# Performance work log

Hardware: AMD Instinct MI355X
Metric: run time of the kernel (lower is better)

The kernel has to match this reference:

```python
import jax, jax.numpy as jnp
import numpy as np

B, I, H = 8192, 1024, 1024


def setup_inputs() -> dict:
    key = jax.random.key(0)
    k1, k2, k3, k4, k5 = jax.random.split(key, 5)
    bound_in = 1.0 / np.sqrt(I)
    return {
        "input": jax.random.normal(k1, (B, I), dtype=jnp.float32),
        "weights": jax.random.uniform(k2, (4 * H, H + I), dtype=jnp.float32, minval=-bound_in, maxval=bound_in),
        "bias": jax.random.uniform(k3, (4 * H,), dtype=jnp.float32, minval=-bound_in, maxval=bound_in),
        "old_h": jax.random.normal(k4, (B, H), dtype=jnp.float32),
        "old_cell": jax.random.normal(k5, (B, H), dtype=jnp.float32),
    }


def reference(input, weights, bias, old_h, old_cell):
    # X = [old_h, input] matches weights = cat(recurrent_W, input_W, dim=1)
    X = jnp.concatenate([old_h, input], axis=1)            # [B, H+I]
    gates = jax.nn.sigmoid(X @ weights.T + bias)           # [B, 4H], all gates sigmoid
    in_g, out_g, z_g, f_g = jnp.split(gates, 4, axis=1)    # each [B, H]
    new_cell = old_cell * f_g + z_g - in_g                 # subtractive cell update
    new_h = jax.nn.sigmoid(new_cell) - out_g               # subtractive output
    return new_h, new_cell
```

## Files before the change

kernel.cpp:

```cpp
#include <hip/hip_runtime.h>
#include <hip/hip_bf16.h>

namespace {

constexpr int kB = 8192;
constexpr int kH = 1024;
constexpr int kK = 2048;
constexpr int kG = 4 * kH;

typedef float f32x4 __attribute__((ext_vector_type(4)));
typedef unsigned short u16x8 __attribute__((ext_vector_type(8)));

__device__ __forceinline__ unsigned short f2bf(float f) {
  return __builtin_bit_cast(unsigned short, __float2bfloat16(f));
}
__device__ __forceinline__ float sigmoidf_(float x) {
  return 1.0f / (1.0f + __expf(-x));
}
__device__ __forceinline__ u16x8 pack8(const float4 v0, const float4 v1) {
  return u16x8{f2bf(v0.x), f2bf(v0.y), f2bf(v0.z), f2bf(v0.w),
               f2bf(v1.x), f2bf(v1.y), f2bf(v1.z), f2bf(v1.w)};
}

__global__ __launch_bounds__(256) void prep_pack(
    const float* __restrict__ input, const float* __restrict__ weights,
    const float* __restrict__ bias, const float* __restrict__ old_h,
    unsigned short* __restrict__ Aw, unsigned short* __restrict__ Ww,
    float* __restrict__ bias_i) {
  const int b = blockIdx.x;
  const int tid = threadIdx.x;

  if (b >= 3072) {
    const int base = (b - 3072) * 2048 + tid * 8;
    #pragma unroll
    for (int e = 0; e < 8; ++e) {
      const int j = base + e;
      bias_i[j] = bias[(j & 3) * kH + (j >> 2)];
    }
    return;
  }

  __shared__ unsigned short tile[8192];

  const bool isW = (b >= 2048);
  const int tileid = isW ? (b - 2048) : b;
  const int kt  = tileid & 31;
  const int blk = tileid >> 5;

  const int r    = tid >> 1;
  const int half = tid & 1;
  const int k0   = kt * 64 + half * 32;

  const float* src;
  if (!isW) {
    const int row = blk * 128 + r;
    src = (k0 < kH) ? (old_h + (long)row * kH + k0)
                    : (input + (long)row * kH + (k0 - kH));
  } else {
    const int j = blk * 128 + r;
    const int g = j & 3, h = j >> 2;
    src = weights + ((long)g * kH + h) * kK + k0;
  }

  float4 v[8];
  const float4* s4 = (const float4*)src;
  #pragma unroll
  for (int q = 0; q < 8; ++q) v[q] = s4[q];

  const int mb = r >> 4, r15 = r & 15;
  #pragma unroll
  for (int lh = 0; lh < 4; ++lh) {
    const int dst = mb * 1024 + half * 512 + (lh * 16 + r15) * 8;
    *(u16x8*)&tile[dst] = pack8(v[2 * lh], v[2 * lh + 1]);
  }
  __syncthreads();

  unsigned short* out = (isW ? Ww : Aw) + (long)tileid * 8192;
  #pragma unroll
  for (int q = 0; q < 4; ++q)
    *(u16x8*)(out + q * 2048 + tid * 8) = *(const u16x8*)&tile[q * 2048 + tid * 8];
}

__global__ __launch_bounds__(256, 2) void sublstm_gemm(
    const unsigned short* __restrict__ Aw, const unsigned short* __restrict__ Ww,
    const float* __restrict__ bias_i, const float* __restrict__ old_cell,
    float* __restrict__ out) {

  __shared__ union SM {
    struct { unsigned short A0[8192]; unsigned short B0[8192];
             unsigned short A1[8192]; unsigned short B1[8192]; } t;
    float Gc[32][132];
  } sm;
  __shared__ float bias_s[128];

  const int tid  = threadIdx.x;
  const int lane = tid & 63;
  const int wid  = tid >> 6;
  const int wr   = wid >> 1;
  const int wc   = wid & 1;

  const int bid = blockIdx.x;
  const int swz = (bid & 7) * 256 + (bid >> 3);
  const int bm  = swz & 63;
  const int hb  = swz >> 6;

  if (tid < 128) bias_s[tid] = bias_i[hb * 128 + tid];

  const unsigned short* atile = Aw + ((long)bm * 32) * 8192;
  const unsigned short* btile = Ww + ((long)hb * 32) * 8192;
  const int soff = tid * 8;

  unsigned short* A0 = sm.t.A0; unsigned short* B0 = sm.t.B0;
  unsigned short* A1 = sm.t.A1; unsigned short* B1 = sm.t.B1;

  f32x4 acc[4][4];
  #pragma unroll
  for (int m = 0; m < 4; ++m)
    #pragma unroll
    for (int n = 0; n < 4; ++n)
      acc[m][n] = f32x4{0.f, 0.f, 0.f, 0.f};

#define STAGE(LA, LB, KT) do {                                                     \
    const unsigned short* asrc_ = atile + (long)(KT) * 8192 + soff;                \
    const unsigned short* bsrc_ = btile + (long)(KT) * 8192 + soff;                \
    _Pragma("unroll")                                                              \
    for (int i_ = 0; i_ < 4; ++i_) {                                               \
      __builtin_amdgcn_global_load_lds(                                            \
          (const __attribute__((address_space(1))) unsigned int*)(asrc_ + i_ * 2048), \
          (__attribute__((address_space(3))) unsigned int*)((LA) + i_ * 2048 + wid * 512), \
          16, 0, 0);                                                               \
      __builtin_amdgcn_global_load_lds(                                            \
          (const __attribute__((address_space(1))) unsigned int*)(bsrc_ + i_ * 2048), \
          (__attribute__((address_space(3))) unsigned int*)((LB) + i_ * 2048 + wid * 512), \
          16, 0, 0);                                                               \
    }                                                                              \
  } while (0)

#define COMPUTE(LA, LB) do {                                                       \
    _Pragma("unroll")                                                              \
    for (int kk_ = 0; kk_ < 2; ++kk_) {                                            \
      u16x8 af_[4], bf_[4];                                                        \
      _Pragma("unroll")                                                            \
      for (int m_ = 0; m_ < 4; ++m_)                                               \
        af_[m_] = *(const u16x8*)&(LA)[((wr * 4 + m_) * 2 + kk_) * 512 + lane * 8];\
      _Pragma("unroll")                                                            \
      for (int n_ = 0; n_ < 4; ++n_)                                               \
        bf_[n_] = *(const u16x8*)&(LB)[((wc * 4 + n_) * 2 + kk_) * 512 + lane * 8];\
      _Pragma("unroll")                                                            \
      for (int m_ = 0; m_ < 4; ++m_)                                               \
        _Pragma("unroll")                                                          \
        for (int n_ = 0; n_ < 4; ++n_)                                             \
          asm("v_mfma_f32_16x16x32_bf16 %0, %1, %2, %0"                            \
              : "+v"(acc[m_][n_]) : "v"(af_[m_]), "v"(bf_[n_]));                   \
    }                                                                              \
  } while (0)

  STAGE(A0, B0, 0);
  __syncthreads();

  for (int kt = 0; kt + 2 < 32; kt += 2) {
    STAGE(A1, B1, kt + 1);
    COMPUTE(A0, B0);
    __syncthreads();
    STAGE(A0, B0, kt + 2);
    COMPUTE(A1, B1);
    __syncthreads();
  }
  STAGE(A1, B1, 31);

  float ocp[4][4];
  #pragma unroll
  for (int m = 0; m < 4; ++m)
    #pragma unroll
    for (int q = 0; q < 4; ++q) {
      const int r = (tid >> 5) + q * 8;
      const int grow = bm * 128 + (r >> 4) * 64 + m * 16 + (r & 15);
      ocp[m][q] = old_cell[(long)grow * kH + hb * 32 + (tid & 31)];
    }

  COMPUTE(A0, B0);
  __syncthreads();
  COMPUTE(A1, B1);

#undef STAGE
#undef COMPUTE

  float* out_h = out;
  float* out_c = out + (long)kB * kH;

  #pragma unroll
  for (int m = 0; m < 4; ++m) {
    __syncthreads();
    #pragma unroll
    for (int n = 0; n < 4; ++n) {
      const int col = wc * 64 + n * 16 + (lane & 15);
      #pragma unroll
      for (int j = 0; j < 4; ++j)
        sm.Gc[wr * 16 + (lane >> 4) * 4 + j][col] = acc[m][n][j];
    }
    __syncthreads();

    #pragma unroll
    for (int q = 0; q < 4; ++q) {
      const int r = (tid >> 5) + q * 8;
      const int h = tid & 31;
      const float4 gv = *(const float4*)&sm.Gc[r][h * 4];
      const float4 bv = *(const float4*)&bias_s[h * 4];
      const float gi = sigmoidf_(gv.x + bv.x);
      const float go = sigmoidf_(gv.y + bv.y);
      const float gz = sigmoidf_(gv.z + bv.z);
      const float gf = sigmoidf_(gv.w + bv.w);
      const int grow = bm * 128 + (r >> 4) * 64 + m * 16 + (r & 15);
      const long off = (long)grow * kH + hb * 32 + h;
      const float nc = ocp[m][q] * gf + gz - gi;
      out_h[off] = sigmoidf_(nc) - go;
      out_c[off] = nc;
    }
  }
}

constexpr int FBM = 128, FBH = 32, FBN = 128, FBK = 32, FNKT = kK / FBK;

__global__ __launch_bounds__(256, 2) void sublstm_fused(
    const float* __restrict__ input, const float* __restrict__ weights,
    const float* __restrict__ bias, const float* __restrict__ old_h,
    const float* __restrict__ old_cell, float* __restrict__ out) {
  __shared__ unsigned short As[FBM][FBK + 8];
  __shared__ unsigned short Bs[FBN][FBK + 8];
  __shared__ float Gc[32][FBN + 4];

  const int tid = threadIdx.x, lane = tid & 63, wid = tid >> 6;
  const int wr = wid >> 1, wc = wid & 1;
  const int bid = blockIdx.x;
  const int bm = bid & 63, hh0 = (bid >> 6) * FBH;

  const int ra = tid >> 1, ca = (tid & 1) << 4;
  const long arow = (long)bm * FBM + ra;
  const int wrow = (ra >> 5) * kH + hh0 + (ra & 31);
  const float* abase_h = old_h + arow * kH + ca;
  const float* abase_x = input + arow * kH + ca - kH;
  const float* wbase = weights + (long)wrow * kK + ca;

  const int fr = lane & 15, ks = (lane >> 4) << 3;
  f32x4 acc[4][4];
  #pragma unroll
  for (int m = 0; m < 4; ++m)
    #pragma unroll
    for (int n = 0; n < 4; ++n) acc[m][n] = f32x4{0.f, 0.f, 0.f, 0.f};

  float4 a0, a1, a2, a3, b0, b1, b2, b3;
  {
    const float4* ap4 = (const float4*)abase_h;
    const float4* wp4 = (const float4*)wbase;
    a0 = ap4[0]; a1 = ap4[1]; a2 = ap4[2]; a3 = ap4[3];
    b0 = wp4[0]; b1 = wp4[1]; b2 = wp4[2]; b3 = wp4[3];
  }
  for (int kt = 0; kt < FNKT; ++kt) {
    u16x8 pa0 = pack8(a0, a1), pa1 = pack8(a2, a3);
    u16x8 pb0 = pack8(b0, b1), pb1 = pack8(b2, b3);
    __syncthreads();
    *(u16x8*)&As[ra][ca] = pa0; *(u16x8*)&As[ra][ca + 8] = pa1;
    *(u16x8*)&Bs[ra][ca] = pb0; *(u16x8*)&Bs[ra][ca + 8] = pb1;
    __syncthreads();
    if (kt + 1 < FNKT) {
      const int k0n = (kt + 1) * FBK;
      const float* ap = (k0n < kH) ? (abase_h + k0n) : (abase_x + k0n);
      const float4* ap4 = (const float4*)ap;
      const float4* wp4 = (const float4*)(wbase + k0n);
      a0 = ap4[0]; a1 = ap4[1]; a2 = ap4[2]; a3 = ap4[3];
      b0 = wp4[0]; b1 = wp4[1]; b2 = wp4[2]; b3 = wp4[3];
    }
    u16x8 af[4], bfv[4];
    #pragma unroll
    for (int m = 0; m < 4; ++m) af[m] = *(const u16x8*)&As[wr * 64 + m * 16 + fr][ks];
    #pragma unroll
    for (int n = 0; n < 4; ++n) bfv[n] = *(const u16x8*)&Bs[wc * 64 + n * 16 + fr][ks];
    #pragma unroll
    for (int m = 0; m < 4; ++m)
      #pragma unroll
      for (int n = 0; n < 4; ++n)
        asm("v_mfma_f32_16x16x32_bf16 %0, %1, %2, %0"
            : "+v"(acc[m][n]) : "v"(af[m]), "v"(bfv[n]));
  }
  float* out_h = out;
  float* out_c = out + (long)kB * kH;
  #pragma unroll
  for (int m = 0; m < 4; ++m) {
    __syncthreads();
    #pragma unroll
    for (int n = 0; n < 4; ++n) {
      const int col = wc * 64 + n * 16 + fr;
      #pragma unroll
      for (int j = 0; j < 4; ++j)
        Gc[wr * 16 + (lane >> 4) * 4 + j][col] = acc[m][n][j];
    }
    __syncthreads();
    #pragma unroll
    for (int q = 0; q < 4; ++q) {
      const int idx = tid + (q << 8);
      const int r = idx >> 5, h = idx & 31;
      const int hg = hh0 + h;
      const float gi = sigmoidf_(Gc[r][h] + bias[hg]);
      const float go = sigmoidf_(Gc[r][32 + h] + bias[kH + hg]);
      const float gz = sigmoidf_(Gc[r][64 + h] + bias[2 * kH + hg]);
      const float gf = sigmoidf_(Gc[r][96 + h] + bias[3 * kH + hg]);
      const int grow = bm * FBM + (r >> 4) * 64 + m * 16 + (r & 15);
      const long off = (long)grow * kH + hg;
      const float oc = old_cell[off];
      const float nc = oc * gf + gz - gi;
      out_h[off] = sigmoidf_(nc) - go;
      out_c[off] = nc;
    }
  }
}

}

extern "C" void kernel_launch(void* const* d_in, const int* in_sizes, int n_in,
                              void* d_out, int out_size, void* d_ws, size_t ws_size,
                              hipStream_t stream) {
  const float* input    = (const float*)d_in[0];
  const float* weights  = (const float*)d_in[1];
  const float* bias     = (const float*)d_in[2];
  const float* old_h    = (const float*)d_in[3];
  const float* old_cell = (const float*)d_in[4];
  float* out = (float*)d_out;

  const size_t needA = (size_t)kB * kK * 2;
  const size_t needW = (size_t)kG * kK * 2;
  const size_t needBias = (size_t)kG * 4;

  if (ws_size >= needA + needW + needBias) {
    unsigned short* Aw = (unsigned short*)d_ws;
    unsigned short* Ww = (unsigned short*)((char*)d_ws + needA);
    float* bias_i = (float*)((char*)d_ws + needA + needW);
    prep_pack<<<dim3(3074), dim3(256), 0, stream>>>(input, weights, bias, old_h,
                                                    Aw, Ww, bias_i);
    sublstm_gemm<<<dim3(2048), dim3(256), 0, stream>>>(Aw, Ww, bias_i, old_cell, out);
  } else {
    sublstm_fused<<<dim3(2048), dim3(256), 0, stream>>>(input, weights, bias, old_h,
                                                        old_cell, out);
  }
}
```

Measured before the change: 335.6 us.

## Enlarge GEMM tile to 256x256 with 512 threads and restructure packing kernel

The main GEMM moves from 128x128 tiles with 256 threads to 256x256 tiles with 512 threads (8 waves, 8x4 MFMA accumulators per wave). This halves global traffic per FLOP and improves operand reuse from LDS. The prep kernel now has each block process a 128x256 strip with coalesced row reads through a padded LDS buffer, then writes four packed tiles. The epilogue prefetches old_cell one chunk ahead. The cost is higher register pressure (128 accumulator VGPRs) and 128KB of LDS per block, which limits occupancy, and only 512 blocks are launched.

```diff
diff --git a/kernel.cpp b/kernel.cpp
--- a/kernel.cpp
+++ b/kernel.cpp
@@ -10,6 +10,7 @@
 
 typedef float f32x4 __attribute__((ext_vector_type(4)));
 typedef unsigned short u16x8 __attribute__((ext_vector_type(8)));
+typedef unsigned short u16x4 __attribute__((ext_vector_type(4)));
 
 __device__ __forceinline__ unsigned short f2bf(float f) {
   return __builtin_bit_cast(unsigned short, __float2bfloat16(f));
@@ -17,9 +18,8 @@
 __device__ __forceinline__ float sigmoidf_(float x) {
   return 1.0f / (1.0f + __expf(-x));
 }
-__device__ __forceinline__ u16x8 pack8(const float4 v0, const float4 v1) {
-  return u16x8{f2bf(v0.x), f2bf(v0.y), f2bf(v0.z), f2bf(v0.w),
-               f2bf(v1.x), f2bf(v1.y), f2bf(v1.z), f2bf(v1.w)};
+__device__ __forceinline__ u16x4 pack4(const float4 v) {
+  return u16x4{f2bf(v.x), f2bf(v.y), f2bf(v.z), f2bf(v.w)};
 }
 
 __global__ __launch_bounds__(256) void prep_pack(
@@ -30,8 +30,8 @@
   const int b = blockIdx.x;
   const int tid = threadIdx.x;
 
-  if (b >= 3072) {
-    const int base = (b - 3072) * 2048 + tid * 8;
+  if (b >= 768) {
+    const int base = (b - 768) * 2048 + tid * 8;
     #pragma unroll
     for (int e = 0; e < 8; ++e) {
       const int j = base + e;
@@ -40,98 +40,107 @@
     return;
   }
 
-  __shared__ unsigned short tile[8192];
-
-  const bool isW = (b >= 2048);
-  const int tileid = isW ? (b - 2048) : b;
-  const int kt  = tileid & 31;
-  const int blk = tileid >> 5;
-
-  const int r    = tid >> 1;
-  const int half = tid & 1;
-  const int k0   = kt * 64 + half * 32;
-
-  const float* src;
-  if (!isW) {
-    const int row = blk * 128 + r;
-    src = (k0 < kH) ? (old_h + (long)row * kH + k0)
-                    : (input + (long)row * kH + (k0 - kH));
-  } else {
-    const int j = blk * 128 + r;
-    const int g = j & 3, h = j >> 2;
-    src = weights + ((long)g * kH + h) * kK + k0;
-  }
-
-  float4 v[8];
-  const float4* s4 = (const float4*)src;
-  #pragma unroll
-  for (int q = 0; q < 8; ++q) v[q] = s4[q];
-
-  const int mb = r >> 4, r15 = r & 15;
-  #pragma unroll
-  for (int lh = 0; lh < 4; ++lh) {
-    const int dst = mb * 1024 + half * 512 + (lh * 16 + r15) * 8;
-    *(u16x8*)&tile[dst] = pack8(v[2 * lh], v[2 * lh + 1]);
+  __shared__ unsigned short lbuf[128 * 280];
+
+  const int wid = tid >> 6, lane = tid & 63;
+  const bool isW = (b >= 512);
+  const int blk = isW ? (b - 512) : b;
+  const int rb = blk >> 3;
+  const int kc = blk & 7;
+
+  #pragma unroll
+  for (int io = 0; io < 4; ++io) {
+    float4 v[8];
+    #pragma unroll
+    for (int ii = 0; ii < 8; ++ii) {
+      const int row = (io * 8 + ii) * 4 + wid;
+      const float* base;
+      if (!isW) {
+        const long rowg = (long)rb * 128 + row;
+        base = (kc < 4) ? (old_h + rowg * kH + kc * 256)
+                        : (input + rowg * kH + (kc * 256 - kH));
+      } else {
+        const int j = rb * 128 + row;
+        const int g = j & 3, h = j >> 2;
+        base = weights + ((long)g * kH + h) * kK + kc * 256;
+      }
+      v[ii] = ((const float4*)base)[lane];
+    }
+    #pragma unroll
+    for (int ii = 0; ii < 8; ++ii) {
+      const int row = (io * 8 + ii) * 4 + wid;
+      *(u16x4*)&lbuf[row * 280 + lane * 4] = pack4(v[ii]);
+    }
   }
   __syncthreads();
 
-  unsigned short* out = (isW ? Ww : Aw) + (long)tileid * 8192;
-  #pragma unroll
-  for (int q = 0; q < 4; ++q)
-    *(u16x8*)(out + q * 2048 + tid * 8) = *(const u16x8*)&tile[q * 2048 + tid * 8];
-}
-
-__global__ __launch_bounds__(256, 2) void sublstm_gemm(
+  unsigned short* dst = (isW ? Ww : Aw) + ((long)rb * 32 + kc * 4) * 8192;
+  #pragma unroll
+  for (int it = 0; it < 16; ++it) {
+    const int o = (it * 256 + tid) * 8;
+    const int oo = o & 8191;
+    const int tl = o >> 13;
+    const int r15 = (oo >> 3) & 15;
+    const int lh = (oo >> 7) & 3;
+    const int kb = (oo >> 9) & 1;
+    const int mb = oo >> 10;
+    const int row = mb * 16 + r15;
+    const int cs = tl * 64 + kb * 32 + lh * 8;
+    *(u16x8*)(dst + o) = *(const u16x8*)&lbuf[row * 280 + cs];
+  }
+}
+
+__global__ __launch_bounds__(512, 2) void sublstm_gemm(
     const unsigned short* __restrict__ Aw, const unsigned short* __restrict__ Ww,
     const float* __restrict__ bias_i, const float* __restrict__ old_cell,
     float* __restrict__ out) {
 
   __shared__ union SM {
-    struct { unsigned short A0[8192]; unsigned short B0[8192];
-             unsigned short A1[8192]; unsigned short B1[8192]; } t;
-    float Gc[32][132];
+    struct { unsigned short A0[16384]; unsigned short B0[16384];
+             unsigned short A1[16384]; unsigned short B1[16384]; } t;
+    float Gc[32][260];
   } sm;
-  __shared__ float bias_s[128];
+  __shared__ float bias_s[256];
 
   const int tid  = threadIdx.x;
   const int lane = tid & 63;
   const int wid  = tid >> 6;
-  const int wr   = wid >> 1;
-  const int wc   = wid & 1;
+  const int wr   = wid >> 2;
+  const int wc   = wid & 3;
 
   const int bid = blockIdx.x;
-  const int swz = (bid & 7) * 256 + (bid >> 3);
-  const int bm  = swz & 63;
-  const int hb  = swz >> 6;
-
-  if (tid < 128) bias_s[tid] = bias_i[hb * 128 + tid];
-
-  const unsigned short* atile = Aw + ((long)bm * 32) * 8192;
-  const unsigned short* btile = Ww + ((long)hb * 32) * 8192;
-  const int soff = tid * 8;
+  const int swz = (bid & 7) * 64 + (bid >> 3);
+  const int xc  = swz >> 6;
+  const int i6  = swz & 63;
+  const int bm  = (i6 >> 2) * 2 + (i6 & 1);
+  const int hb  = xc * 2 + ((i6 >> 1) & 1);
+
+  if (tid < 256) bias_s[tid] = bias_i[hb * 256 + tid];
 
   unsigned short* A0 = sm.t.A0; unsigned short* B0 = sm.t.B0;
   unsigned short* A1 = sm.t.A1; unsigned short* B1 = sm.t.B1;
 
-  f32x4 acc[4][4];
-  #pragma unroll
-  for (int m = 0; m < 4; ++m)
+  f32x4 acc[8][4];
+  #pragma unroll
+  for (int m = 0; m < 8; ++m)
     #pragma unroll
     for (int n = 0; n < 4; ++n)
       acc[m][n] = f32x4{0.f, 0.f, 0.f, 0.f};
 
 #define STAGE(LA, LB, KT) do {                                                     \
-    const unsigned short* asrc_ = atile + (long)(KT) * 8192 + soff;                \
-    const unsigned short* bsrc_ = btile + (long)(KT) * 8192 + soff;                \
     _Pragma("unroll")                                                              \
     for (int i_ = 0; i_ < 4; ++i_) {                                               \
       __builtin_amdgcn_global_load_lds(                                            \
-          (const __attribute__((address_space(1))) unsigned int*)(asrc_ + i_ * 2048), \
-          (__attribute__((address_space(3))) unsigned int*)((LA) + i_ * 2048 + wid * 512), \
+          (const __attribute__((address_space(1))) unsigned int*)(                 \
+              Aw + ((long)((2 * bm + (i_ >> 1)) * 32 + (KT))) * 8192               \
+                 + (i_ & 1) * 4096 + tid * 8),                                     \
+          (__attribute__((address_space(3))) unsigned int*)((LA) + i_ * 4096 + tid * 8), \
           16, 0, 0);                                                               \
       __builtin_amdgcn_global_load_lds(                                            \
-          (const __attribute__((address_space(1))) unsigned int*)(bsrc_ + i_ * 2048), \
-          (__attribute__((address_space(3))) unsigned int*)((LB) + i_ * 2048 + wid * 512), \
+          (const __attribute__((address_space(1))) unsigned int*)(                 \
+              Ww + ((long)((2 * hb + (i_ >> 1)) * 32 + (KT))) * 8192               \
+                 + (i_ & 1) * 4096 + tid * 8),                                     \
+          (__attribute__((address_space(3))) unsigned int*)((LB) + i_ * 4096 + tid * 8), \
           16, 0, 0);                                                               \
     }                                                                              \
   } while (0)
@@ -139,19 +148,19 @@
 #define COMPUTE(LA, LB) do {                                                       \
     _Pragma("unroll")                                                              \
     for (int kk_ = 0; kk_ < 2; ++kk_) {                                            \
-      u16x8 af_[4], bf_[4];                                                        \
-      _Pragma("unroll")                                                            \
-      for (int m_ = 0; m_ < 4; ++m_)                                               \
-        af_[m_] = *(const u16x8*)&(LA)[((wr * 4 + m_) * 2 + kk_) * 512 + lane * 8];\
+      u16x8 bf_[4];                                                                \
       _Pragma("unroll")                                                            \
       for (int n_ = 0; n_ < 4; ++n_)                                               \
-        bf_[n_] = *(const u16x8*)&(LB)[((wc * 4 + n_) * 2 + kk_) * 512 + lane * 8];\
+        bf_[n_] = *(const u16x8*)&(LB)[(wc >> 1) * 8192 + ((wc & 1) * 4 + n_) * 1024 \
+                                        + kk_ * 512 + lane * 8];                   \
       _Pragma("unroll")                                                            \
-      for (int m_ = 0; m_ < 4; ++m_)                                               \
+      for (int m_ = 0; m_ < 8; ++m_) {                                             \
+        u16x8 af_ = *(const u16x8*)&(LA)[wr * 8192 + m_ * 1024 + kk_ * 512 + lane * 8]; \
         _Pragma("unroll")                                                          \
         for (int n_ = 0; n_ < 4; ++n_)                                             \
           asm("v_mfma_f32_16x16x32_bf16 %0, %1, %2, %0"                            \
-              : "+v"(acc[m_][n_]) : "v"(af_[m_]), "v"(bf_[n_]));                   \
+              : "+v"(acc[m_][n_]) : "v"(af_), "v"(bf_[n_]));                       \
+      }                                                                            \
     }                                                                              \
   } while (0)
 
@@ -168,15 +177,12 @@
   }
   STAGE(A1, B1, 31);
 
-  float ocp[4][4];
-  #pragma unroll
-  for (int m = 0; m < 4; ++m)
-    #pragma unroll
-    for (int q = 0; q < 4; ++q) {
-      const int r = (tid >> 5) + q * 8;
-      const int grow = bm * 128 + (r >> 4) * 64 + m * 16 + (r & 15);
-      ocp[m][q] = old_cell[(long)grow * kH + hb * 32 + (tid & 31)];
-    }
+  float cnx[4];
+  #pragma unroll
+  for (int q = 0; q < 4; ++q) {
+    const int grow = bm * 256 + q * 8 + wid;
+    cnx[q] = old_cell[(long)grow * kH + hb * 64 + lane];
+  }
 
   COMPUTE(A0, B0);
   __syncthreads();
@@ -189,30 +195,47 @@
   float* out_c = out + (long)kB * kH;
 
   #pragma unroll
-  for (int m = 0; m < 4; ++m) {
-    __syncthreads();
-    #pragma unroll
-    for (int n = 0; n < 4; ++n) {
-      const int col = wc * 64 + n * 16 + (lane & 15);
+  for (int c = 0; c < 8; ++c) {
+    const int wrc = c >> 2, mm = c & 3;
+    __syncthreads();
+    if (wr == wrc) {
       #pragma unroll
-      for (int j = 0; j < 4; ++j)
-        sm.Gc[wr * 16 + (lane >> 4) * 4 + j][col] = acc[m][n][j];
-    }
-    __syncthreads();
+      for (int m2 = 0; m2 < 2; ++m2)
+        #pragma unroll
+        for (int n = 0; n < 4; ++n) {
+          const int col = wc * 64 + n * 16 + (lane & 15);
+          const int rb_ = m2 * 16 + (lane >> 4) * 4;
+          #pragma unroll
+          for (int j = 0; j < 4; ++j)
+            sm.Gc[rb_ + j][col] = acc[mm * 2 + m2][n][j];
+        }
+    }
+    __syncthreads();
+
+    float cc[4];
+    #pragma unroll
+    for (int q = 0; q < 4; ++q) cc[q] = cnx[q];
+    if (c < 7) {
+      const int c2 = c + 1;
+      #pragma unroll
+      for (int q = 0; q < 4; ++q) {
+        const int grow = bm * 256 + (c2 >> 2) * 128 + (c2 & 3) * 32 + q * 8 + wid;
+        cnx[q] = old_cell[(long)grow * kH + hb * 64 + lane];
+      }
+    }
 
     #pragma unroll
     for (int q = 0; q < 4; ++q) {
-      const int r = (tid >> 5) + q * 8;
-      const int h = tid & 31;
-      const float4 gv = *(const float4*)&sm.Gc[r][h * 4];
-      const float4 bv = *(const float4*)&bias_s[h * 4];
+      const int r = q * 8 + wid;
+      const float4 gv = *(const float4*)&sm.Gc[r][lane * 4];
+      const float4 bv = *(const float4*)&bias_s[lane * 4];
       const float gi = sigmoidf_(gv.x + bv.x);
       const float go = sigmoidf_(gv.y + bv.y);
       const float gz = sigmoidf_(gv.z + bv.z);
       const float gf = sigmoidf_(gv.w + bv.w);
-      const int grow = bm * 128 + (r >> 4) * 64 + m * 16 + (r & 15);
-      const long off = (long)grow * kH + hb * 32 + h;
-      const float nc = ocp[m][q] * gf + gz - gi;
+      const int grow = bm * 256 + wrc * 128 + mm * 32 + r;
+      const long off = (long)grow * kH + hb * 64 + lane;
+      const float nc = cc[q] * gf + gz - gi;
       out_h[off] = sigmoidf_(nc) - go;
       out_c[off] = nc;
     }
@@ -220,6 +243,11 @@
 }
 
 constexpr int FBM = 128, FBH = 32, FBN = 128, FBK = 32, FNKT = kK / FBK;
+
+__device__ __forceinline__ u16x8 pack8f(const float4 v0, const float4 v1) {
+  return u16x8{f2bf(v0.x), f2bf(v0.y), f2bf(v0.z), f2bf(v0.w),
+               f2bf(v1.x), f2bf(v1.y), f2bf(v1.z), f2bf(v1.w)};
+}
 
 __global__ __launch_bounds__(256, 2) void sublstm_fused(
     const float* __restrict__ input, const float* __restrict__ weights,
@@ -256,8 +284,8 @@
     b0 = wp4[0]; b1 = wp4[1]; b2 = wp4[2]; b3 = wp4[3];
   }
   for (int kt = 0; kt < FNKT; ++kt) {
-    u16x8 pa0 = pack8(a0, a1), pa1 = pack8(a2, a3);
-    u16x8 pb0 = pack8(b0, b1), pb1 = pack8(b2, b3);
+    u16x8 pa0 = pack8f(a0, a1), pa1 = pack8f(a2, a3);
+    u16x8 pb0 = pack8f(b0, b1), pb1 = pack8f(b2, b3);
     __syncthreads();
     *(u16x8*)&As[ra][ca] = pa0; *(u16x8*)&As[ra][ca + 8] = pa1;
     *(u16x8*)&Bs[ra][ca] = pb0; *(u16x8*)&Bs[ra][ca + 8] = pb1;
@@ -334,9 +362,9 @@
     unsigned short* Aw = (unsigned short*)d_ws;
     unsigned short* Ww = (unsigned short*)((char*)d_ws + needA);
     float* bias_i = (float*)((char*)d_ws + needA + needW);
-    prep_pack<<<dim3(3074), dim3(256), 0, stream>>>(input, weights, bias, old_h,
-                                                    Aw, Ww, bias_i);
-    sublstm_gemm<<<dim3(2048), dim3(256), 0, stream>>>(Aw, Ww, bias_i, old_cell, out);
+    prep_pack<<<dim3(770), dim3(256), 0, stream>>>(input, weights, bias, old_h,
+                                                   Aw, Ww, bias_i);
+    sublstm_gemm<<<dim3(512), dim3(512), 0, stream>>>(Aw, Ww, bias_i, old_cell, out);
   } else {
     sublstm_fused<<<dim3(2048), dim3(256), 0, stream>>>(input, weights, bias, old_h,
                                                         old_cell, out);
```

After: 317.1 us. 1.06x faster.
